# Kernel tuning notes

Measured on AMD Instinct MI355X. Metric: run time of the kernel, lower is better.

Reference implementation:

```python
import jax, jax.numpy as jnp
import numpy as np

V, D, G = 128000, 2048, 32  # vocab, embedding dim, int4 group size
B, S = 8, 4096
QMIN, QMAX = -8, 7  # int4 range (bit_width=4)


def setup_inputs() -> dict:
    key = jax.random.key(0)
    k1, k2, k3, k4 = jax.random.split(key, 4)
    # int4 values stored in int8-like container: range [-8, 7]
    weight = jax.random.randint(k1, (V, D), 0, 16, dtype=jnp.int32) - 8
    scale = jax.random.uniform(k2, (V, D // G), dtype=jnp.float32) * 0.02 + 1e-3
    zero_point = jax.random.randint(k3, (V, D // G), 0, 16, dtype=jnp.int32) - 8
    x = jax.random.randint(k4, (B, S), 0, V, dtype=jnp.int64)
    return {"weight": weight, "scale": scale, "zero_point": zero_point, "x": x}


def reference(weight, scale, zero_point, x):
    # Group-wise dequant: (w - zero_point) * scale, per group of G channels,
    # matching _quantized_decomposed_dequantize_per_channel_group.
    n_groups = scale.shape[1]
    g = weight.shape[1] // n_groups  # group_size
    w = weight.reshape(weight.shape[0], n_groups, g).astype(scale.dtype)
    zp = zero_point.reshape(zero_point.shape[0], n_groups, 1).astype(scale.dtype)
    w_dq = ((w - zp) * scale[:, :, None]).reshape(weight.shape)  # [V, D]
    # F.embedding with padding_idx=None, max_norm=None is a plain gather
    return w_dq[x]  # [B, S, D]
```

## Files before the change

### kernel.cpp

```cpp
#include <hip/hip_runtime.h>


#define DIM 2048
#define NGROUPS 64

typedef float  f32x4 __attribute__((ext_vector_type(4)));
typedef int    i32x4 __attribute__((ext_vector_type(4)));

__global__ __launch_bounds__(256) void int4_embed_dequant_kernel(
    const int* __restrict__ weight,
    const float* __restrict__ scale,
    const int* __restrict__ zp,
    const int* __restrict__ x,
    float* __restrict__ out,
    int n_tokens)
{
    const int t = threadIdx.x;
    const int g = t >> 2;
    const int stride = gridDim.x;

    int token = blockIdx.x;
    if (token >= n_tokens) return;

    int row = x[token];

    while (token < n_tokens) {
        const int next_token = token + stride;
        int next_row = 0;
        if (next_token < n_tokens) next_row = x[next_token];

        const size_t srow = (size_t)row * NGROUPS + g;
        const float s = scale[srow];
        const float z = (float)zp[srow];

        const i32x4* __restrict__ wrow =
            (const i32x4*)weight + (size_t)row * (DIM / 4) + (t << 1);
        f32x4* orow =
            (f32x4*)out + (size_t)token * (DIM / 4) + (t << 1);

        const i32x4 w0 = wrow[0];
        const i32x4 w1 = wrow[1];

        f32x4 o0, o1;
        o0.x = ((float)w0.x - z) * s;
        o0.y = ((float)w0.y - z) * s;
        o0.z = ((float)w0.z - z) * s;
        o0.w = ((float)w0.w - z) * s;
        o1.x = ((float)w1.x - z) * s;
        o1.y = ((float)w1.y - z) * s;
        o1.z = ((float)w1.z - z) * s;
        o1.w = ((float)w1.w - z) * s;

        __builtin_nontemporal_store(o0, orow);
        __builtin_nontemporal_store(o1, orow + 1);

        token = next_token;
        row = next_row;
    }
}

extern "C" void kernel_launch(void* const* d_in, const int* in_sizes, int n_in,
                              void* d_out, int out_size, void* d_ws, size_t ws_size,
                              hipStream_t stream) {
    const int* weight  = (const int*)d_in[0];
    const float* scale = (const float*)d_in[1];
    const int* zp      = (const int*)d_in[2];
    const int* x       = (const int*)d_in[3];

    float* out = (float*)d_out;

    const int n_tokens = in_sizes[3];

    int grid = 2048;
    if (grid > n_tokens) grid = n_tokens;

    int4_embed_dequant_kernel<<<dim3(grid), dim3(256), 0, stream>>>(
        weight, scale, zp, x, out, n_tokens);
}
```

Before: 98.68 us.

## Assign one wavefront per token row with shuffled scale/zero-point broadcast

Switches from one 256-thread block per token to one 64-lane wavefront per token. Each lane issues eight strided 16-byte weight loads, so more loads are in flight at once. Each lane loads one group's scale and zero point, and __shfl broadcasts them to the lanes that need them. The intent is to raise memory-level parallelism and reduce redundant scale loads. The cost is extra register pressure and shuffle instructions, and each wave now handles four times as many tokens in the grid-stride loop.

Measured after the change: 88.41 us. 1.12x faster.

```diff
diff --git a/kernel.cpp b/kernel.cpp
--- a/kernel.cpp
+++ b/kernel.cpp
@@ -2,7 +2,6 @@
 
 
 #define DIM 2048
-#define NGROUPS 64
 
 typedef float  f32x4 __attribute__((ext_vector_type(4)));
 typedef int    i32x4 __attribute__((ext_vector_type(4)));
@@ -15,47 +14,44 @@
     float* __restrict__ out,
     int n_tokens)
 {
-    const int t = threadIdx.x;
-    const int g = t >> 2;
-    const int stride = gridDim.x;
+    const int lane = threadIdx.x & 63;
+    const int wid  = (blockIdx.x << 2) + (threadIdx.x >> 6);
+    const int nw   = gridDim.x << 2;
 
-    int token = blockIdx.x;
-    if (token >= n_tokens) return;
+    int tok = wid;
+    if (tok >= n_tokens) return;
+    int row = x[tok];
 
-    int row = x[token];
+    while (tok < n_tokens) {
+        const int ntok = tok + nw;
+        const int nrow = (ntok < n_tokens) ? x[ntok] : 0;
 
-    while (token < n_tokens) {
-        const int next_token = token + stride;
-        int next_row = 0;
-        if (next_token < n_tokens) next_row = x[next_token];
+        const size_t sbase = (size_t)row * 64 + lane;
+        const float s_my = scale[sbase];
+        const float z_my = (float)zp[sbase];
 
-        const size_t srow = (size_t)row * NGROUPS + g;
-        const float s = scale[srow];
-        const float z = (float)zp[srow];
+        const i32x4* __restrict__ wr =
+            (const i32x4*)weight + (size_t)row * (DIM / 4) + lane;
+        i32x4 wv[8];
+#pragma unroll
+        for (int k = 0; k < 8; ++k) wv[k] = wr[k * 64];
 
-        const i32x4* __restrict__ wrow =
-            (const i32x4*)weight + (size_t)row * (DIM / 4) + (t << 1);
-        f32x4* orow =
-            (f32x4*)out + (size_t)token * (DIM / 4) + (t << 1);
+        f32x4* orow = (f32x4*)out + (size_t)tok * (DIM / 4) + lane;
+#pragma unroll
+        for (int k = 0; k < 8; ++k) {
+            const int src = (k << 3) + (lane >> 3);
+            const float sk = __shfl(s_my, src);
+            const float zk = __shfl(z_my, src);
+            f32x4 o;
+            o.x = ((float)wv[k].x - zk) * sk;
+            o.y = ((float)wv[k].y - zk) * sk;
+            o.z = ((float)wv[k].z - zk) * sk;
+            o.w = ((float)wv[k].w - zk) * sk;
+            __builtin_nontemporal_store(o, orow + k * 64);
+        }
 
-        const i32x4 w0 = wrow[0];
-        const i32x4 w1 = wrow[1];
-
-        f32x4 o0, o1;
-        o0.x = ((float)w0.x - z) * s;
-        o0.y = ((float)w0.y - z) * s;
-        o0.z = ((float)w0.z - z) * s;
-        o0.w = ((float)w0.w - z) * s;
-        o1.x = ((float)w1.x - z) * s;
-        o1.y = ((float)w1.y - z) * s;
-        o1.z = ((float)w1.z - z) * s;
-        o1.w = ((float)w1.w - z) * s;
-
-        __builtin_nontemporal_store(o0, orow);
-        __builtin_nontemporal_store(o1, orow + 1);
-
-        token = next_token;
-        row = next_row;
+        tok = ntok;
+        row = nrow;
     }
 }
 
@@ -72,7 +68,8 @@
     const int n_tokens = in_sizes[3];
 
     int grid = 2048;
-    if (grid > n_tokens) grid = n_tokens;
+    int needed = (n_tokens + 3) / 4;
+    if (grid > needed) grid = needed;
 
     int4_embed_dequant_kernel<<<dim3(grid), dim3(256), 0, stream>>>(
         weight, scale, zp, x, out, n_tokens);
```
